# Optimization experiments

Hardware: AMD Instinct MI355X
Metric: run time of the kernel (lower is better)

## Reference

```python
import jax, jax.numpy as jnp
import numpy as np

N_HEAD = 16
R = 4  # reciprocal rank

def setup_inputs() -> dict:
    key = jax.random.key(0)
    ks = jax.random.split(key, 8)
    B, T, C = 2, 2048, 1024
    H = N_HEAD
    D = C // H
    D_std = D - R
    x = jax.random.normal(ks[0], (B, T, C), dtype=jnp.float32)
    W_attn = jax.random.normal(ks[1], (3 * C, C), dtype=jnp.float32) * (1.0 / np.sqrt(C))
    W_proj = jax.random.normal(ks[2], (C, C), dtype=jnp.float32) * (1.0 / np.sqrt(C))
    w_std = jnp.full((H,), D_std / D, dtype=jnp.float32)
    w_rec = jnp.full((H,), R / D, dtype=jnp.float32)
    skip_std = jnp.float32(2.0)
    skip_low = jnp.float32(-3.0)
    rwr_alpha = jnp.full((H,), 0.05, dtype=jnp.float32)
    return {"x": x, "W_attn": W_attn, "W_proj": W_proj, "w_std": w_std,
            "w_rec": w_rec, "skip_std": skip_std, "skip_low": skip_low,
            "rwr_alpha": rwr_alpha}

def reference(x, W_attn, W_proj, w_std, w_rec, skip_std, skip_low, rwr_alpha):
    B, T, C = x.shape
    H = N_HEAD
    D = C // H
    D_std = D - R
    # fused QKV projection: [Qf | Kf | V]
    fused = jnp.einsum('btc,fc->btf', x, W_attn)
    qf, kf, v = jnp.split(fused, 3, axis=-1)
    Qf = qf.reshape(B, T, H, D).transpose(0, 2, 1, 3)  # (B,H,T,D)
    Kf = kf.reshape(B, T, H, D).transpose(0, 2, 1, 3)
    V = v.reshape(B, T, H, D).transpose(0, 2, 1, 3)
    # dynamic per-head gate scaling folded into Qf/Kf
    g_std = jnp.sqrt(jnp.clip(w_std * jax.nn.sigmoid(skip_std), 1e-8))  # (H,)
    g_rec = jnp.sqrt(jnp.clip(w_rec * jax.nn.sigmoid(skip_low), 1e-8))  # (H,)
    scale = jnp.concatenate([
        jnp.broadcast_to(g_std[:, None], (H, D_std)),
        jnp.broadcast_to(g_rec[:, None], (H, R)),
    ], axis=-1)  # (H, D)
    scale = scale[None, :, None, :]  # (1,H,1,D)
    Qf = Qf * scale
    Kf = Kf * scale
    # causal SDPA (scale = 1/sqrt(head_dim), dropout=0)
    scores = jnp.einsum('bhqd,bhkd->bhqk', Qf, Kf) / jnp.sqrt(jnp.float32(D))
    causal = jnp.tril(jnp.ones((T, T), dtype=bool))
    scores = jnp.where(causal[None, None], scores, jnp.float32(-1e30))
    attn = jax.nn.softmax(scores, axis=-1)
    y = jnp.einsum('bhqk,bhkd->bhqd', attn, V)
    # self-restart mix: out = (1-alpha)*attn_out + alpha*V, alpha in [0, 0.5]
    alpha = jnp.clip(rwr_alpha, 0.0, 0.5)[None, :, None, None]
    y = (1.0 - alpha) * y + alpha * V
    y = y.transpose(0, 2, 1, 3).reshape(B, T, C)
    return jnp.einsum('btc,oc->bto', y, W_proj)
```

## Files before the change

### kernel.cpp

```cpp
#include <hip/hip_runtime.h>
#include <hip/hip_bf16.h>
#include <math.h>
#include <stdint.h>

#define B_    2
#define T_    2048
#define C_    1024
#define H_    16
#define D_    64
#define R_    4
#define DSTD  60
#define F_    3072
#define BT_   (B_ * T_)

#define LOG2E 1.44269504088896340736f

typedef __bf16 bf16x8 __attribute__((ext_vector_type(8)));
typedef __bf16 bf16x4 __attribute__((ext_vector_type(4)));
typedef float  f32x4  __attribute__((ext_vector_type(4)));

__device__ __forceinline__ int swz(int row, int blk) {
    return blk ^ ((row >> 1) & 7);
}

__device__ __forceinline__ void st_pair(__bf16* p, __bf16 a, __bf16 b) {
    union { __bf16 h[2]; uint32_t u; } t;
    t.h[0] = a; t.h[1] = b;
    *(uint32_t*)p = t.u;
}

__device__ __forceinline__ void gload_lds16(const void* g, void* l) {
    __builtin_amdgcn_global_load_lds(
        (const __attribute__((address_space(1))) uint32_t*)g,
        (__attribute__((address_space(3))) uint32_t*)l, 16, 0, 0);
}

__global__ __launch_bounds__(256) void cast3_kernel(
    const float* __restrict__ a, int na4,
    const float* __restrict__ b, int nb4,
    const float* __restrict__ c, int nc4,
    __bf16* __restrict__ oa, __bf16* __restrict__ ob, __bf16* __restrict__ oc)
{
    int i = blockIdx.x * 256 + threadIdx.x;
    const float* s; __bf16* d; int j = i;
    if (j < na4) { s = a; d = oa; }
    else {
        j -= na4;
        if (j < nb4) { s = b; d = ob; }
        else {
            j -= nb4;
            if (j >= nc4) return;
            s = c; d = oc;
        }
    }
    float4 v = ((const float4*)s)[j];
    bf16x4 o;
    o[0] = (__bf16)v.x; o[1] = (__bf16)v.y;
    o[2] = (__bf16)v.z; o[3] = (__bf16)v.w;
    ((bf16x4*)d)[j] = o;
}

__global__ __launch_bounds__(256) void gemm_qkv_kernel(
    const __bf16* __restrict__ A,
    const __bf16* __restrict__ Bw,
    const float* __restrict__ w_std, const float* __restrict__ w_rec,
    const float* __restrict__ skip_std, const float* __restrict__ skip_low,
    __bf16* __restrict__ Q, __bf16* __restrict__ K, __bf16* __restrict__ V)
{
    __shared__ __bf16 As[128 * 64];
    __shared__ __bf16 Bs[128 * 64];

    const int tid  = threadIdx.x;
    const int row0 = blockIdx.x * 128;
    const int col0 = blockIdx.y * 128;

    const int w    = tid >> 6;
    const int lane = tid & 63;
    const int quad = lane >> 4;
    const int lt   = lane & 15;
    const int wm   = w >> 1;
    const int wn   = w & 1;

    const int srow = tid >> 3;
    const int sblk = tid & 7;

    f32x4 acc[4][4];
#pragma unroll
    for (int i = 0; i < 4; ++i)
#pragma unroll
        for (int j = 0; j < 4; ++j)
#pragma unroll
            for (int r = 0; r < 4; ++r) acc[i][j][r] = 0.f;

    for (int kt = 0; kt < C_ / 64; ++kt) {
        const int k0 = kt * 64;
        __syncthreads();
#pragma unroll
        for (int cc = 0; cc < 4; ++cc) {
            const int r  = cc * 32 + srow;
            const int sb = sblk ^ ((r >> 1) & 7);
            gload_lds16(A  + (size_t)(row0 + r) * C_ + k0 + sb * 8,
                        As + cc * 2048 + tid * 8);
            gload_lds16(Bw + (size_t)(col0 + r) * C_ + k0 + sb * 8,
                        Bs + cc * 2048 + tid * 8);
        }
        __syncthreads();

        bf16x8 waf[2][4], xf[2][4];
#pragma unroll
        for (int kk = 0; kk < 2; ++kk)
#pragma unroll
            for (int i = 0; i < 4; ++i) {
                const int rf = wn * 64 + i * 16 + lt;
                waf[kk][i] = *(const bf16x8*)&Bs[rf * 64 + swz(rf, kk * 4 + quad) * 8];
                const int rt = wm * 64 + i * 16 + lt;
                xf[kk][i]  = *(const bf16x8*)&As[rt * 64 + swz(rt, kk * 4 + quad) * 8];
            }
#pragma unroll
        for (int kk = 0; kk < 2; ++kk)
#pragma unroll
            for (int i = 0; i < 4; ++i)
#pragma unroll
                for (int j = 0; j < 4; ++j)
                    acc[i][j] = __builtin_amdgcn_mfma_f32_16x16x32_bf16(
                        waf[kk][i], xf[kk][j], acc[i][j], 0, 0, 0);
    }

    const int colbase = col0 + wn * 64;
    const int which   = colbase >> 10;
    const int h       = (colbase & (C_ - 1)) >> 6;

    const float ss = 1.f / (1.f + __expf(-skip_std[0]));
    const float sl = 1.f / (1.f + __expf(-skip_low[0]));
    const float gs = sqrtf(fmaxf(w_std[h] * ss, 1e-8f));
    const float gr = sqrtf(fmaxf(w_rec[h] * sl, 1e-8f));

    __bf16* dstM = (which == 0) ? Q : (which == 1) ? K : V;

#pragma unroll
    for (int i = 0; i < 4; ++i) {
        const int d0 = i * 16 + quad * 4;
        float sc = (d0 < DSTD) ? gs : gr;
        if (which == 0) sc *= 0.125f * LOG2E;
        const bool scale = (which != 2);
#pragma unroll
        for (int j = 0; j < 4; ++j) {
            const int trow = row0 + wm * 64 + j * 16 + lt;
            const int b = trow >> 11;
            const int t = trow & (T_ - 1);
            bf16x4 o;
#pragma unroll
            for (int r = 0; r < 4; ++r) {
                float v = acc[i][j][r];
                if (scale) v *= sc;
                o[r] = (__bf16)v;
            }
            *(bf16x4*)(dstM + (((size_t)b * H_ + h) * T_ + t) * D_ + d0) = o;
        }
    }
}

__global__ __launch_bounds__(256) void gemm_out_kernel(
    const __bf16* __restrict__ A,
    const __bf16* __restrict__ Bw,
    float* __restrict__ out)
{
    __shared__ __bf16 As[128 * 64];
    __shared__ __bf16 Bs[64 * 64];

    const int tid  = threadIdx.x;
    const int row0 = blockIdx.x * 128;
    const int col0 = blockIdx.y * 64;

    const int w    = tid >> 6;
    const int lane = tid & 63;
    const int quad = lane >> 4;
    const int lt   = lane & 15;
    const int wm   = w >> 1;
    const int wn   = w & 1;

    const int srow = tid >> 3;
    const int sblk = tid & 7;

    f32x4 acc[2][4];
#pragma unroll
    for (int i = 0; i < 2; ++i)
#pragma unroll
        for (int j = 0; j < 4; ++j)
#pragma unroll
            for (int r = 0; r < 4; ++r) acc[i][j][r] = 0.f;

    for (int kt = 0; kt < C_ / 64; ++kt) {
        const int k0 = kt * 64;
        __syncthreads();
#pragma unroll
        for (int cc = 0; cc < 4; ++cc) {
            const int r  = cc * 32 + srow;
            const int sb = sblk ^ ((r >> 1) & 7);
            gload_lds16(A + (size_t)(row0 + r) * C_ + k0 + sb * 8,
                        As + cc * 2048 + tid * 8);
        }
#pragma unroll
        for (int cc = 0; cc < 2; ++cc) {
            const int r  = cc * 32 + srow;
            const int sb = sblk ^ ((r >> 1) & 7);
            gload_lds16(Bw + (size_t)(col0 + r) * C_ + k0 + sb * 8,
                        Bs + cc * 2048 + tid * 8);
        }
        __syncthreads();

        bf16x8 wpf[2][2], yf[2][4];
#pragma unroll
        for (int kk = 0; kk < 2; ++kk) {
#pragma unroll
            for (int i = 0; i < 2; ++i) {
                const int rb = wn * 32 + i * 16 + lt;
                wpf[kk][i] = *(const bf16x8*)&Bs[rb * 64 + swz(rb, kk * 4 + quad) * 8];
            }
#pragma unroll
            for (int j = 0; j < 4; ++j) {
                const int ra = wm * 64 + j * 16 + lt;
                yf[kk][j] = *(const bf16x8*)&As[ra * 64 + swz(ra, kk * 4 + quad) * 8];
            }
        }
#pragma unroll
        for (int kk = 0; kk < 2; ++kk)
#pragma unroll
            for (int i = 0; i < 2; ++i)
#pragma unroll
                for (int j = 0; j < 4; ++j)
                    acc[i][j] = __builtin_amdgcn_mfma_f32_16x16x32_bf16(
                        wpf[kk][i], yf[kk][j], acc[i][j], 0, 0, 0);
    }

#pragma unroll
    for (int i = 0; i < 2; ++i) {
        const int o = col0 + wn * 32 + i * 16 + quad * 4;
#pragma unroll
        for (int j = 0; j < 4; ++j) {
            const int trow = row0 + wm * 64 + j * 16 + lt;
            float4 v;
            v.x = acc[i][j][0]; v.y = acc[i][j][1];
            v.z = acc[i][j][2]; v.w = acc[i][j][3];
            *(float4*)(out + (size_t)trow * C_ + o) = v;
        }
    }
}

__global__ __launch_bounds__(512) void attn_kernel(
    const __bf16* __restrict__ Q, const __bf16* __restrict__ K,
    const __bf16* __restrict__ V, const float* __restrict__ rwr_alpha,
    __bf16* __restrict__ Y)
{
    __shared__ __align__(16) __bf16 Ks[2][64][64];
    __shared__ __align__(16) __bf16 Vt[2][64][64];
    __shared__ __align__(16) __bf16 Ps[8][16][64];

    const int tid = threadIdx.x;
    const int bh  = blockIdx.x & 31;
    const int g   = blockIdx.x >> 5;
    const int qb  = (g < 8) ? (15 - g) : (g - 8);
    const int h   = bh & (H_ - 1);
    const int b   = bh >> 4;

    const __bf16* Qb = Q + (((size_t)b * H_ + h) * T_) * D_;
    const __bf16* Kb = K + (((size_t)b * H_ + h) * T_) * D_;
    const __bf16* Vb = V + (((size_t)b * H_ + h) * T_) * D_;

    const int w    = tid >> 6;
    const int lane = tid & 63;
    const int quad = lane >> 4;
    const int lt   = lane & 15;

    const int kr = tid >> 3;
    const int kc = (tid & 7) ^ ((kr >> 1) & 7);

    const bool vstg = (tid < 256);
    const int kp = (tid >> 3) * 2;
    const int dc = (tid & 7) * 8;
    const int kblk = (kp >> 3) & 7, koff = kp & 7;

    const int ktmax  = 2 * qb + 1;
    const int tile_w = 2 * qb + (w >> 2);

    const __bf16* qrow = Qb + (size_t)(qb * 128 + w * 16 + lt) * D_;
    bf16x8 qf[2];
    qf[0] = *(const bf16x8*)(qrow + quad * 8);
    qf[1] = *(const bf16x8*)(qrow + 32 + quad * 8);

    bf16x8 ones;
#pragma unroll
    for (int u = 0; u < 8; ++u) ones[u] = (__bf16)1.0f;

    gload_lds16(Kb + (size_t)kr * 64 + kc * 8, &Ks[0][0][0] + tid * 8);
    if (vstg) {
        const __bf16* vs = Vb + (size_t)kp * 64 + dc;
        bf16x8 v1 = *(const bf16x8*)(vs);
        bf16x8 v2 = *(const bf16x8*)(vs + 64);
#pragma unroll
        for (int u = 0; u < 8; ++u) {
            const int row = dc + u;
            st_pair(&Vt[0][row][swz(row, kblk) * 8 + koff], v1[u], v2[u]);
        }
    }
    __syncthreads();

    f32x4 lacc;
    f32x4 oacc[4];
#pragma unroll
    for (int r = 0; r < 4; ++r) lacc[r] = 0.f;
#pragma unroll
    for (int n = 0; n < 4; ++n)
#pragma unroll
        for (int r = 0; r < 4; ++r) oacc[n][r] = 0.f;

    for (int kt = 0; kt <= ktmax; ++kt) {
        const int cur = kt & 1;
        const int nxt = 1 - cur;
        const bool pre = (kt < ktmax);

        bf16x8 v1, v2;
        if (pre) {
            const size_t toff = (size_t)(kt + 1) * 4096;
            gload_lds16(Kb + toff + (size_t)kr * 64 + kc * 8,
                        &Ks[nxt][0][0] + tid * 8);
            if (vstg) {
                const __bf16* vs = Vb + toff + (size_t)kp * 64 + dc;
                v1 = *(const bf16x8*)(vs);
                v2 = *(const bf16x8*)(vs + 64);
            }
        }

        if (kt <= tile_w) {
            f32x4 sacc[4];
#pragma unroll
            for (int n = 0; n < 4; ++n)
#pragma unroll
                for (int r = 0; r < 4; ++r) sacc[n][r] = 0.f;
#pragma unroll
            for (int kk = 0; kk < 2; ++kk) {
#pragma unroll
                for (int n = 0; n < 4; ++n) {
                    const int row = n * 16 + lt;
                    bf16x8 ak = *(const bf16x8*)&Ks[cur][row][swz(row, kk * 4 + quad) * 8];
                    sacc[n] = __builtin_amdgcn_mfma_f32_16x16x32_bf16(ak, qf[kk], sacc[n], 0, 0, 0);
                }
            }

            if (kt == tile_w) {
                const int ql = (w & 3) * 16 + lt;
#pragma unroll
                for (int n = 0; n < 4; ++n) {
                    const int keyb = n * 16 + quad * 4;
#pragma unroll
                    for (int r = 0; r < 4; ++r)
                        if (keyb + r > ql) sacc[n][r] = -1e30f;
                }
            }

#pragma unroll
            for (int n = 0; n < 4; ++n) {
                bf16x4 pv;
#pragma unroll
                for (int r = 0; r < 4; ++r)
                    pv[r] = (__bf16)__builtin_amdgcn_exp2f(sacc[n][r]);
                *(bf16x4*)&Ps[w][lt][swz(lt, n * 2 + (quad >> 1)) * 8 + (quad & 1) * 4] = pv;
            }

#pragma unroll
            for (int kk = 0; kk < 2; ++kk) {
                bf16x8 ap = *(const bf16x8*)&Ps[w][lt][swz(lt, kk * 4 + quad) * 8];
                lacc = __builtin_amdgcn_mfma_f32_16x16x32_bf16(ap, ones, lacc, 0, 0, 0);
#pragma unroll
                for (int nd = 0; nd < 4; ++nd) {
                    const int drow = nd * 16 + lt;
                    bf16x8 bv = *(const bf16x8*)&Vt[cur][drow][swz(drow, kk * 4 + quad) * 8];
                    oacc[nd] = __builtin_amdgcn_mfma_f32_16x16x32_bf16(ap, bv, oacc[nd], 0, 0, 0);
                }
            }

            {
                const float lm = fmaxf(fmaxf(lacc[0], lacc[1]), fmaxf(lacc[2], lacc[3]));
                if (__ballot(lm > 1.0e12f)) {
                    const float sc = 1.0f / 4294967296.0f;
#pragma unroll
                    for (int r = 0; r < 4; ++r) lacc[r] *= sc;
#pragma unroll
                    for (int n = 0; n < 4; ++n)
#pragma unroll
                        for (int r = 0; r < 4; ++r) oacc[n][r] *= sc;
                }
            }
        }

        if (pre && vstg) {
#pragma unroll
            for (int u = 0; u < 8; ++u) {
                const int row = dc + u;
                st_pair(&Vt[nxt][row][swz(row, kblk) * 8 + koff], v1[u], v2[u]);
            }
        }
        __syncthreads();
    }

    const float a = fminf(fmaxf(rwr_alpha[h], 0.f), 0.5f);
#pragma unroll
    for (int r = 0; r < 4; ++r) {
        const float inv = 1.f / lacc[r];
        const int qg = qb * 128 + w * 16 + quad * 4 + r;
        const __bf16* vp = Vb + (size_t)qg * D_;
        __bf16* yp = Y + ((size_t)(b * T_ + qg)) * C_ + h * D_;
#pragma unroll
        for (int nd = 0; nd < 4; ++nd) {
            const int d = nd * 16 + lt;
            yp[d] = (__bf16)((1.f - a) * oacc[nd][r] * inv + a * (float)vp[d]);
        }
    }
}

extern "C" void kernel_launch(void* const* d_in, const int* in_sizes, int n_in,
                              void* d_out, int out_size, void* d_ws, size_t ws_size,
                              hipStream_t stream) {
    const float* x        = (const float*)d_in[0];
    const float* W_attn   = (const float*)d_in[1];
    const float* W_proj   = (const float*)d_in[2];
    const float* w_std    = (const float*)d_in[3];
    const float* w_rec    = (const float*)d_in[4];
    const float* skip_std = (const float*)d_in[5];
    const float* skip_low = (const float*)d_in[6];
    const float* rwr      = (const float*)d_in[7];
    float* out = (float*)d_out;

    const size_t nX  = (size_t)BT_ * C_;
    const size_t nWa = (size_t)F_ * C_;
    const size_t nWp = (size_t)C_ * C_;
    const size_t per = (size_t)B_ * H_ * T_ * D_;

    __bf16* xb  = (__bf16*)d_ws;
    __bf16* Wab = xb  + nX;
    __bf16* Wpb = Wab + nWa;
    __bf16* Qb  = Wpb + nWp;
    __bf16* Kb  = Qb  + per;
    __bf16* Vb  = Kb  + per;
    __bf16* Yb  = Vb  + per;

    const int na4 = nX / 4, nb4 = nWa / 4, nc4 = nWp / 4;
    cast3_kernel<<<dim3((na4 + nb4 + nc4 + 255) / 256), 256, 0, stream>>>(
        x, na4, W_attn, nb4, W_proj, nc4, xb, Wab, Wpb);

    gemm_qkv_kernel<<<dim3(BT_ / 128, F_ / 128), 256, 0, stream>>>(
        xb, Wab, w_std, w_rec, skip_std, skip_low, Qb, Kb, Vb);
    attn_kernel<<<dim3(16 * 32), 512, 0, stream>>>(Qb, Kb, Vb, rwr, Yb);
    gemm_out_kernel<<<dim3(BT_ / 128, C_ / 64), 256, 0, stream>>>(Yb, Wpb, out);
}
```

Measured before the change: 178.0 us.

## Double-buffer LDS tiles in QKV and output projection GEMMs

Both projection GEMMs now use two LDS buffers. The next K-tile's global-to-LDS loads are issued before the MFMA work on the current tile, with one barrier per iteration instead of two. The aim is to hide global load latency behind the matrix math. In exchange, LDS use per block doubles, which may lower occupancy. The async global_load_lds writes also depend on waitcnt and barrier semantics to be correct.

```diff
diff --git a/kernel.cpp b/kernel.cpp
--- a/kernel.cpp
+++ b/kernel.cpp
@@ -67,8 +67,8 @@
     const float* __restrict__ skip_std, const float* __restrict__ skip_low,
     __bf16* __restrict__ Q, __bf16* __restrict__ K, __bf16* __restrict__ V)
 {
-    __shared__ __bf16 As[128 * 64];
-    __shared__ __bf16 Bs[128 * 64];
+    __shared__ __bf16 As[2][128 * 64];
+    __shared__ __bf16 Bs[2][128 * 64];
 
     const int tid  = threadIdx.x;
     const int row0 = blockIdx.x * 128;
@@ -92,19 +92,31 @@
 #pragma unroll
             for (int r = 0; r < 4; ++r) acc[i][j][r] = 0.f;
 
+#pragma unroll
+    for (int cc = 0; cc < 4; ++cc) {
+        const int r  = cc * 32 + srow;
+        const int sb = sblk ^ ((r >> 1) & 7);
+        gload_lds16(A  + (size_t)(row0 + r) * C_ + sb * 8,
+                    &As[0][cc * 2048 + tid * 8]);
+        gload_lds16(Bw + (size_t)(col0 + r) * C_ + sb * 8,
+                    &Bs[0][cc * 2048 + tid * 8]);
+    }
+    __syncthreads();
+
     for (int kt = 0; kt < C_ / 64; ++kt) {
-        const int k0 = kt * 64;
-        __syncthreads();
-#pragma unroll
-        for (int cc = 0; cc < 4; ++cc) {
-            const int r  = cc * 32 + srow;
-            const int sb = sblk ^ ((r >> 1) & 7);
-            gload_lds16(A  + (size_t)(row0 + r) * C_ + k0 + sb * 8,
-                        As + cc * 2048 + tid * 8);
-            gload_lds16(Bw + (size_t)(col0 + r) * C_ + k0 + sb * 8,
-                        Bs + cc * 2048 + tid * 8);
-        }
-        __syncthreads();
+        const int cur = kt & 1;
+        if (kt + 1 < C_ / 64) {
+            const int k0 = (kt + 1) * 64;
+#pragma unroll
+            for (int cc = 0; cc < 4; ++cc) {
+                const int r  = cc * 32 + srow;
+                const int sb = sblk ^ ((r >> 1) & 7);
+                gload_lds16(A  + (size_t)(row0 + r) * C_ + k0 + sb * 8,
+                            &As[cur ^ 1][cc * 2048 + tid * 8]);
+                gload_lds16(Bw + (size_t)(col0 + r) * C_ + k0 + sb * 8,
+                            &Bs[cur ^ 1][cc * 2048 + tid * 8]);
+            }
+        }
 
         bf16x8 waf[2][4], xf[2][4];
 #pragma unroll
@@ -112,9 +124,9 @@
 #pragma unroll
             for (int i = 0; i < 4; ++i) {
                 const int rf = wn * 64 + i * 16 + lt;
-                waf[kk][i] = *(const bf16x8*)&Bs[rf * 64 + swz(rf, kk * 4 + quad) * 8];
+                waf[kk][i] = *(const bf16x8*)&Bs[cur][rf * 64 + swz(rf, kk * 4 + quad) * 8];
                 const int rt = wm * 64 + i * 16 + lt;
-                xf[kk][i]  = *(const bf16x8*)&As[rt * 64 + swz(rt, kk * 4 + quad) * 8];
+                xf[kk][i]  = *(const bf16x8*)&As[cur][rt * 64 + swz(rt, kk * 4 + quad) * 8];
             }
 #pragma unroll
         for (int kk = 0; kk < 2; ++kk)
@@ -124,6 +136,7 @@
                 for (int j = 0; j < 4; ++j)
                     acc[i][j] = __builtin_amdgcn_mfma_f32_16x16x32_bf16(
                         waf[kk][i], xf[kk][j], acc[i][j], 0, 0, 0);
+        __syncthreads();
     }
 
     const int colbase = col0 + wn * 64;
@@ -165,8 +178,8 @@
     const __bf16* __restrict__ Bw,
     float* __restrict__ out)
 {
-    __shared__ __bf16 As[128 * 64];
-    __shared__ __bf16 Bs[64 * 64];
+    __shared__ __bf16 As[2][128 * 64];
+    __shared__ __bf16 Bs[2][64 * 64];
 
     const int tid  = threadIdx.x;
     const int row0 = blockIdx.x * 128;
@@ -190,24 +203,41 @@
 #pragma unroll
             for (int r = 0; r < 4; ++r) acc[i][j][r] = 0.f;
 
+#pragma unroll
+    for (int cc = 0; cc < 4; ++cc) {
+        const int r  = cc * 32 + srow;
+        const int sb = sblk ^ ((r >> 1) & 7);
+        gload_lds16(A + (size_t)(row0 + r) * C_ + sb * 8,
+                    &As[0][cc * 2048 + tid * 8]);
+    }
+#pragma unroll
+    for (int cc = 0; cc < 2; ++cc) {
+        const int r  = cc * 32 + srow;
+        const int sb = sblk ^ ((r >> 1) & 7);
+        gload_lds16(Bw + (size_t)(col0 + r) * C_ + sb * 8,
+                    &Bs[0][cc * 2048 + tid * 8]);
+    }
+    __syncthreads();
+
     for (int kt = 0; kt < C_ / 64; ++kt) {
-        const int k0 = kt * 64;
-        __syncthreads();
-#pragma unroll
-        for (int cc = 0; cc < 4; ++cc) {
-            const int r  = cc * 32 + srow;
-            const int sb = sblk ^ ((r >> 1) & 7);
-            gload_lds16(A + (size_t)(row0 + r) * C_ + k0 + sb * 8,
-                        As + cc * 2048 + tid * 8);
-        }
-#pragma unroll
-        for (int cc = 0; cc < 2; ++cc) {
-            const int r  = cc * 32 + srow;
-            const int sb = sblk ^ ((r >> 1) & 7);
-            gload_lds16(Bw + (size_t)(col0 + r) * C_ + k0 + sb * 8,
-                        Bs + cc * 2048 + tid * 8);
-        }
-        __syncthreads();
+        const int cur = kt & 1;
+        if (kt + 1 < C_ / 64) {
+            const int k0 = (kt + 1) * 64;
+#pragma unroll
+            for (int cc = 0; cc < 4; ++cc) {
+                const int r  = cc * 32 + srow;
+                const int sb = sblk ^ ((r >> 1) & 7);
+                gload_lds16(A + (size_t)(row0 + r) * C_ + k0 + sb * 8,
+                            &As[cur ^ 1][cc * 2048 + tid * 8]);
+            }
+#pragma unroll
+            for (int cc = 0; cc < 2; ++cc) {
+                const int r  = cc * 32 + srow;
+                const int sb = sblk ^ ((r >> 1) & 7);
+                gload_lds16(Bw + (size_t)(col0 + r) * C_ + k0 + sb * 8,
+                            &Bs[cur ^ 1][cc * 2048 + tid * 8]);
+            }
+        }
 
         bf16x8 wpf[2][2], yf[2][4];
 #pragma unroll
@@ -215,12 +245,12 @@
 #pragma unroll
             for (int i = 0; i < 2; ++i) {
                 const int rb = wn * 32 + i * 16 + lt;
-                wpf[kk][i] = *(const bf16x8*)&Bs[rb * 64 + swz(rb, kk * 4 + quad) * 8];
+                wpf[kk][i] = *(const bf16x8*)&Bs[cur][rb * 64 + swz(rb, kk * 4 + quad) * 8];
             }
 #pragma unroll
             for (int j = 0; j < 4; ++j) {
                 const int ra = wm * 64 + j * 16 + lt;
-                yf[kk][j] = *(const bf16x8*)&As[ra * 64 + swz(ra, kk * 4 + quad) * 8];
+                yf[kk][j] = *(const bf16x8*)&As[cur][ra * 64 + swz(ra, kk * 4 + quad) * 8];
             }
         }
 #pragma unroll
@@ -231,6 +261,7 @@
                 for (int j = 0; j < 4; ++j)
                     acc[i][j] = __builtin_amdgcn_mfma_f32_16x16x32_bf16(
                         wpf[kk][i], yf[kk][j], acc[i][j], 0, 0, 0);
+        __syncthreads();
     }
 
 #pragma unroll
```

New measurement: 185.6 us. 4.3% more time.
